# Performance work log

Measured on AMD Instinct MI355X. Metric: run time of the kernel, lower is better.

## Reference

```python
import jax, jax.numpy as jnp
import numpy as np

C = 128          # hidden_channels
N = 50000        # num nodes
E = 600000       # num edges
G = 256          # num graphs
PI = 3.141592653589793
EPS = 1e-5       # BatchNorm eps


def _lin(key, fan_in, fan_out):
    return jax.random.normal(key, (fan_in, fan_out), jnp.float32) / jnp.sqrt(fan_in)


def setup_inputs() -> dict:
    key = jax.random.key(0)
    ks = jax.random.split(key, 40)
    inp = {}
    inp["x"] = jax.random.normal(ks[0], (N, C), jnp.float32)
    inp["edge_index"] = jax.random.randint(ks[1], (2, E), 0, N)
    inp["edge_attr"] = jax.random.normal(ks[2], (E, C), jnp.float32)
    inp["batch"] = jnp.sort(jax.random.randint(ks[3], (N,), 0, G))
    # GATv2Conv 1
    inp["Wl1"] = _lin(ks[4], C, C); inp["bl1"] = jnp.zeros((C,), jnp.float32)
    inp["Wr1"] = _lin(ks[5], C, C); inp["br1"] = jnp.zeros((C,), jnp.float32)
    inp["We1"] = _lin(ks[6], C, C)
    inp["att1"] = jax.random.normal(ks[7], (C,), jnp.float32) / jnp.sqrt(C)
    inp["bo1"] = jnp.zeros((C,), jnp.float32)
    # GATv2Conv 2
    inp["Wl2"] = _lin(ks[8], C, C); inp["bl2"] = jnp.zeros((C,), jnp.float32)
    inp["Wr2"] = _lin(ks[9], C, C); inp["br2"] = jnp.zeros((C,), jnp.float32)
    inp["We2"] = _lin(ks[10], C, C)
    inp["att2"] = jax.random.normal(ks[11], (C,), jnp.float32) / jnp.sqrt(C)
    inp["bo2"] = jnp.zeros((C,), jnp.float32)
    # BatchNorms (affine)
    inp["g1"] = jnp.ones((C,), jnp.float32); inp["be1"] = jnp.zeros((C,), jnp.float32)
    inp["g2"] = jnp.ones((C,), jnp.float32); inp["be2"] = jnp.zeros((C,), jnp.float32)
    # AttentionalAggregation gate MLP (lin1 -> tanh -> lin2)
    inp["Ag1"] = _lin(ks[12], C, C); inp["bg1"] = jnp.zeros((C,), jnp.float32)
    inp["Ag2"] = _lin(ks[13], C, C); inp["bg2"] = jnp.zeros((C,), jnp.float32)
    # final Linear
    inp["Wf"] = _lin(ks[14], C, C); inp["bf"] = jnp.zeros((C,), jnp.float32)
    return inp


def gatv2(x, src, dst, ea, Wl, bl, Wr, br, We, att, bo):
    # add self-loops with fill_value='mean' (mean of incoming edge_attr per node)
    ones = jnp.ones(src.shape, x.dtype)
    deg = jax.ops.segment_sum(ones, dst, N)
    loop_attr = jax.ops.segment_sum(ea, dst, N) / jnp.maximum(deg, 1.0)[:, None]
    ar = jnp.arange(N)
    s = jnp.concatenate([src, ar])
    d = jnp.concatenate([dst, ar])
    ea_full = jnp.concatenate([ea, loop_attr], axis=0)  # [E+N, C]
    xl = x @ Wl + bl   # source transform
    xr = x @ Wr + br   # target transform
    m = xl[s] + xr[d] + ea_full @ We                    # [E+N, C]
    a = jnp.sum(jax.nn.leaky_relu(m, 0.2) * att, axis=-1)  # [E+N]
    # scatter-softmax over incoming edges of each target node
    amax = jax.ops.segment_max(a, d, N)
    ex = jnp.exp(a - amax[d])
    den = jax.ops.segment_sum(ex, d, N)
    alpha = ex / den[d]
    return jax.ops.segment_sum(alpha[:, None] * xl[s], d, N) + bo


def batchnorm(x, g, b):
    mu = x.mean(axis=0)
    var = x.var(axis=0)
    return (x - mu) * jax.lax.rsqrt(var + EPS) * g + b


def att_pool(x, batch, A1, b1, A2, b2):
    # gate_nn: lin1 -> tanh -> lin2, then per-graph per-feature softmax weights
    gate = jnp.tanh(x @ A1 + b1) @ A2 + b2              # [N, C]
    gmax = jax.ops.segment_max(gate, batch, G)
    eg = jnp.exp(gate - gmax[batch])
    den = jax.ops.segment_sum(eg, batch, G)
    w = eg / den[batch]
    return jax.ops.segment_sum(w * x, batch, G)          # [G, C]


def reference(x, edge_index, edge_attr, batch,
              Wl1, bl1, Wr1, br1, We1, att1, bo1,
              Wl2, bl2, Wr2, br2, We2, att2, bo2,
              g1, be1, g2, be2,
              Ag1, bg1, Ag2, bg2, Wf, bf):
    src, dst = edge_index[0], edge_index[1]
    h = gatv2(x, src, dst, edge_attr, Wl1, bl1, Wr1, br1, We1, att1, bo1)
    h = jnp.tanh(batchnorm(h, g1, be1))   # dropout = identity (eval)
    h = gatv2(h, src, dst, edge_attr, Wl2, bl2, Wr2, br2, We2, att2, bo2)
    h = jnp.tanh(batchnorm(h, g2, be2))
    p = att_pool(h, batch, Ag1, bg1, Ag2, bg2)           # [G, C]
    o = jnp.tanh(p @ Wf + bf)
    axis, aperture = jnp.split(o, 2, axis=-1)            # [G, C//2] each
    return axis * PI, (aperture + 1.0) * PI
```

## Files before the change

### kernel.cpp

```cpp
#include <hip/hip_runtime.h>
#include <hip/hip_bf16.h>
#include <math.h>

#define C 128
#define NN 50000
#define EE 600000
#define GG 256
#define PI_F 3.14159265358979323846f
#define EPS_BN 1e-5f
#define SCAN_G ((NN + 255) / 256)

typedef __attribute__((ext_vector_type(8)))  short  short8;
typedef __attribute__((ext_vector_type(16))) float  floatx16;
typedef __attribute__((ext_vector_type(4)))  float  float4v;
typedef __attribute__((ext_vector_type(4)))  unsigned short ushort4v;

static __device__ __forceinline__ short f2bs(float x) {
    union { float f; unsigned u; } v; v.f = x;
    unsigned r = v.u + 0x7FFF + ((v.u >> 16) & 1);
    return (short)(r >> 16);
}
static __device__ __forceinline__ float bs2f(unsigned short b) {
    union { unsigned u; float f; } v; v.u = (unsigned)b << 16; return v.f;
}

__global__ void k_cast(const float* __restrict__ in, unsigned short* __restrict__ out, int n4) {
    int i = blockIdx.x * blockDim.x + threadIdx.x;
    if (i < n4) {
        float4v v = ((const float4v*)in)[i];
        ushort4v o;
        o.x = (unsigned short)f2bs(v.x); o.y = (unsigned short)f2bs(v.y);
        o.z = (unsigned short)f2bs(v.z); o.w = (unsigned short)f2bs(v.w);
        ((ushort4v*)out)[i] = o;
    }
}

__global__ void k_prep(const float* __restrict__ W0, const float* __restrict__ W1,
                       const float* __restrict__ W2, const float* __restrict__ W3,
                       const float* __restrict__ W4, const float* __restrict__ W5,
                       const float* __restrict__ W6, const float* __restrict__ W7,
                       unsigned short* __restrict__ WT) {
    __shared__ short s[C * 136];
    const float* W;
    switch (blockIdx.x) {
        case 0: W = W0; break; case 1: W = W1; break;
        case 2: W = W2; break; case 3: W = W3; break;
        case 4: W = W4; break; case 5: W = W5; break;
        case 6: W = W6; break; default: W = W7; break;
    }
    for (int i = threadIdx.x; i < C * C; i += 256) {
        int k = i >> 7, n = i & (C - 1);
        s[n * 136 + k] = f2bs(W[i]);
    }
    __syncthreads();
    unsigned short* out = WT + (size_t)blockIdx.x * C * C;
    for (int i8 = threadIdx.x; i8 < C * C / 8; i8 += 256) {
        int n = i8 >> 4, k0 = (i8 & 15) * 8;
        *(short8*)(out + n * C + k0) = *(const short8*)&s[n * 136 + k0];
    }
}

static __device__ __forceinline__ void stage_wt(const unsigned short* __restrict__ WT, short* sWT) {
    for (int i8 = threadIdx.x; i8 < C * C / 8; i8 += 256) {
        int n = i8 >> 4, k0 = (i8 & 15) * 8;
        *(short8*)&sWT[n * 136 + k0] = *(const short8*)(WT + n * C + k0);
    }
}

__global__ void k_count(const int* __restrict__ dst, int* __restrict__ deg) {
    int e = blockIdx.x * blockDim.x + threadIdx.x;
    if (e < EE) atomicAdd(&deg[dst[e]], 1);
}

__global__ void k_scan1(const int* __restrict__ deg, int* __restrict__ bsum) {
    __shared__ int s[256];
    int t = threadIdx.x;
    int idx = blockIdx.x * 256 + t;
    s[t] = (idx < NN) ? deg[idx] : 0;
    __syncthreads();
    for (int off = 128; off > 0; off >>= 1) {
        if (t < off) s[t] += s[t + off];
        __syncthreads();
    }
    if (t == 0) bsum[blockIdx.x] = s[0];
}

__global__ void k_scan2(const int* __restrict__ bsum, int* __restrict__ boff, int* __restrict__ row_ptr) {
    __shared__ int s[256];
    int t = threadIdx.x;
    int v0 = (t < SCAN_G) ? bsum[t] : 0;
    s[t] = v0;
    __syncthreads();
    for (int off = 1; off < 256; off <<= 1) {
        int v = (t >= off) ? s[t - off] : 0;
        __syncthreads();
        s[t] += v;
        __syncthreads();
    }
    if (t < SCAN_G) boff[t] = s[t] - v0;
    if (t == 255) row_ptr[NN] = s[255];
}

__global__ void k_scan3(const int* __restrict__ deg, const int* __restrict__ boff,
                        int* __restrict__ row_ptr) {
    __shared__ int s[256];
    int t = threadIdx.x;
    int idx = blockIdx.x * 256 + t;
    int v = (idx < NN) ? deg[idx] : 0;
    s[t] = v;
    __syncthreads();
    for (int off = 1; off < 256; off <<= 1) {
        int u = (t >= off) ? s[t - off] : 0;
        __syncthreads();
        s[t] += u;
        __syncthreads();
    }
    if (idx < NN) row_ptr[idx] = boff[blockIdx.x] + s[t] - v;
}

__global__ void k_fill(const int* __restrict__ src, const int* __restrict__ dst,
                       const int* __restrict__ row_ptr, int* __restrict__ fill,
                       int* __restrict__ eid, int* __restrict__ scsr, int* __restrict__ dcsr) {
    int e = blockIdx.x * blockDim.x + threadIdx.x;
    if (e < EE) {
        int d = dst[e];
        int pos = atomicAdd(&fill[d], 1);
        int i = row_ptr[d] + pos;
        eid[i] = e;
        scsr[i] = src[e];
        dcsr[i] = d;
    }
}

__global__ void k_cast_esum(const float* __restrict__ ea, const int* __restrict__ eid,
                            const int* __restrict__ row_ptr,
                            unsigned short* __restrict__ ea_csr, unsigned short* __restrict__ esum) {
    int n = blockIdx.x; int c = threadIdx.x;
    int s = row_ptr[n], e = row_ptr[n + 1];
    float acc = 0.f;
    for (int i = s; i < e; i++) {
        float v = ea[(size_t)eid[i] * C + c];
        acc += v;
        ea_csr[(size_t)i * C + c] = (unsigned short)f2bs(v);
    }
    esum[(size_t)n * C + c] = (unsigned short)f2bs(acc / fmaxf((float)(e - s), 1.f));
}

template<bool TANH, bool OUT_BF16>
__launch_bounds__(256)
__global__ void k_gemm(const unsigned short* __restrict__ A, const unsigned short* __restrict__ WT,
                       const float* __restrict__ bias, void* __restrict__ outv, int M) {
    __shared__ short sWT[C * 136];
    stage_wt(WT, sWT);
    __syncthreads();

    int lane = threadIdx.x & 63;
    int wave = threadIdx.x >> 6;
    int m    = lane & 31;
    int half = lane >> 5;
    int row0 = blockIdx.x * 128 + wave * 32;
    int rowA = row0 + m;
    int rowC = (rowA < M) ? rowA : (M - 1);
    const unsigned short* rp = A + (size_t)rowC * C;

    floatx16 acc[4];
    #pragma unroll
    for (int t = 0; t < 4; ++t)
        #pragma unroll
        for (int r = 0; r < 16; ++r) acc[t][r] = 0.f;

    #pragma unroll
    for (int s = 0; s < 8; ++s) {
        int k0 = s * 16 + half * 8;
        short8 af = *(const short8*)(rp + k0);
        #pragma unroll
        for (int t = 0; t < 4; ++t) {
            short8 bfr = *(const short8*)(&sWT[(t * 32 + m) * 136 + k0]);
            acc[t] = __builtin_amdgcn_mfma_f32_32x32x16_bf16(af, bfr, acc[t], 0, 0, 0);
        }
    }

    #pragma unroll
    for (int t = 0; t < 4; ++t) {
        int n = t * 32 + m;
        float b = bias ? bias[n] : 0.f;
        #pragma unroll
        for (int r = 0; r < 16; ++r) {
            int rl  = (r & 3) + 8 * (r >> 2) + 4 * half;
            int row = row0 + rl;
            if (row < M) {
                float v = acc[t][r] + b;
                if (TANH) v = tanhf(v);
                if (OUT_BF16) ((unsigned short*)outv)[(size_t)row * C + n] = (unsigned short)f2bs(v);
                else          ((float*)outv)[(size_t)row * C + n] = v;
            }
        }
    }
}

__launch_bounds__(256)
__global__ void k_gemm2(const unsigned short* __restrict__ A,
                        const unsigned short* __restrict__ WT0, const float* __restrict__ b0,
                        const unsigned short* __restrict__ WT1, const float* __restrict__ b1,
                        unsigned short* __restrict__ out0, unsigned short* __restrict__ out1,
                        int M) {
    __shared__ short sWT[C * 136];
    int lane = threadIdx.x & 63;
    int wave = threadIdx.x >> 6;
    int m    = lane & 31;
    int half = lane >> 5;
    int row0 = blockIdx.x * 128 + wave * 32;
    int rowA = row0 + m;
    int rowC = (rowA < M) ? rowA : (M - 1);
    const unsigned short* rp = A + (size_t)rowC * C;

    short8 af[8];
    #pragma unroll
    for (int s = 0; s < 8; ++s) af[s] = *(const short8*)(rp + s * 16 + half * 8);

    for (int phase = 0; phase < 2; ++phase) {
        const unsigned short* WT = phase ? WT1 : WT0;
        const float* bb = phase ? b1 : b0;
        unsigned short* out = phase ? out1 : out0;
        if (phase) __syncthreads();
        stage_wt(WT, sWT);
        __syncthreads();

        floatx16 acc[4];
        #pragma unroll
        for (int t = 0; t < 4; ++t)
            #pragma unroll
            for (int r = 0; r < 16; ++r) acc[t][r] = 0.f;

        #pragma unroll
        for (int s = 0; s < 8; ++s) {
            int k0 = s * 16 + half * 8;
            #pragma unroll
            for (int t = 0; t < 4; ++t) {
                short8 bfr = *(const short8*)(&sWT[(t * 32 + m) * 136 + k0]);
                acc[t] = __builtin_amdgcn_mfma_f32_32x32x16_bf16(af[s], bfr, acc[t], 0, 0, 0);
            }
        }

        #pragma unroll
        for (int t = 0; t < 4; ++t) {
            int n = t * 32 + m;
            float b = bb[n];
            #pragma unroll
            for (int r = 0; r < 16; ++r) {
                int rl  = (r & 3) + 8 * (r >> 2) + 4 * half;
                int row = row0 + rl;
                if (row < M)
                    out[(size_t)row * C + n] = (unsigned short)f2bs(acc[t][r] + b);
            }
        }
    }
}

template<bool SELF>
__launch_bounds__(256)
__global__ void k_gemm_logit(const unsigned short* __restrict__ A, const unsigned short* __restrict__ WT,
                             const unsigned short* __restrict__ xl, const unsigned short* __restrict__ xr,
                             const int* __restrict__ scsr, const int* __restrict__ dcsr,
                             const float* __restrict__ att, float* __restrict__ aout, int M) {
    __shared__ short sWT[C * 136];
    stage_wt(WT, sWT);
    __syncthreads();

    int lane = threadIdx.x & 63;
    int wave = threadIdx.x >> 6;
    int m    = lane & 31;
    int half = lane >> 5;
    int row0 = blockIdx.x * 128 + wave * 32;
    int rowA = row0 + m;
    int rowC = (rowA < M) ? rowA : (M - 1);
    const unsigned short* rp = A + (size_t)rowC * C;

    floatx16 acc[4];
    #pragma unroll
    for (int t = 0; t < 4; ++t)
        #pragma unroll
        for (int r = 0; r < 16; ++r) acc[t][r] = 0.f;

    #pragma unroll
    for (int s = 0; s < 8; ++s) {
        int k0 = s * 16 + half * 8;
        short8 af = *(const short8*)(rp + k0);
        #pragma unroll
        for (int t = 0; t < 4; ++t) {
            short8 bfr = *(const short8*)(&sWT[(t * 32 + m) * 136 + k0]);
            acc[t] = __builtin_amdgcn_mfma_f32_32x32x16_bf16(af, bfr, acc[t], 0, 0, 0);
        }
    }

    float attv[4];
    #pragma unroll
    for (int t = 0; t < 4; ++t) attv[t] = att[t * 32 + m];

    #pragma unroll
    for (int r = 0; r < 16; ++r) {
        int rl  = (r & 3) + 8 * (r >> 2) + 4 * half;
        int row = row0 + rl;
        int rc  = (row < M) ? row : (M - 1);
        int si, di;
        if (SELF) { si = rc; di = rc; }
        else      { si = scsr[rc]; di = dcsr[rc]; }
        const unsigned short* xls = xl + (size_t)si * C;
        const unsigned short* xrs = xr + (size_t)di * C;
        float p = 0.f;
        #pragma unroll
        for (int t = 0; t < 4; ++t) {
            int col = t * 32 + m;
            float v = acc[t][r] + bs2f(xls[col]) + bs2f(xrs[col]);
            v = (v >= 0.f) ? v : 0.2f * v;
            p = fmaf(v, attv[t], p);
        }
        p += __shfl_xor(p, 1);  p += __shfl_xor(p, 2);  p += __shfl_xor(p, 4);
        p += __shfl_xor(p, 8);  p += __shfl_xor(p, 16);
        if (m == 0 && row < M) aout[row] = p;
    }
}

__global__ void k_attn(const unsigned short* __restrict__ xl, const float* __restrict__ a,
                       const int* __restrict__ row_ptr, const int* __restrict__ scsr,
                       const float* __restrict__ bo, float* __restrict__ out) {
    int n = blockIdx.x * 4 + (threadIdx.x >> 6);
    int lane = threadIdx.x & 63;
    if (n >= NN) return;
    int s = row_ptr[n], e = row_ptr[n + 1];
    float aself = a[EE + n];
    float mx = aself;
    for (int i = s + lane; i < e; i += 64) mx = fmaxf(mx, a[i]);
    #pragma unroll
    for (int o = 1; o < 64; o <<= 1) mx = fmaxf(mx, __shfl_xor(mx, o));
    float part = (lane == 0) ? expf(aself - mx) : 0.f;
    for (int i = s + lane; i < e; i += 64) part += expf(a[i] - mx);
    #pragma unroll
    for (int o = 1; o < 64; o <<= 1) part += __shfl_xor(part, o);
    float inv = 1.f / part;

    int sub = lane >> 4;
    int cb  = (lane & 15) * 8;
    float acc[8];
    #pragma unroll
    for (int j = 0; j < 8; ++j) acc[j] = 0.f;

    if (sub == 0) {
        float w = expf(aself - mx) * inv;
        short8 v = *(const short8*)(xl + (size_t)n * C + cb);
        #pragma unroll
        for (int j = 0; j < 8; ++j) acc[j] = w * bs2f((unsigned short)v[j]);
    }

    for (int i = s + sub; i < e; i += 4) {
        float w = expf(a[i] - mx) * inv;
        int sd = scsr[i];
        short8 v = *(const short8*)(xl + (size_t)sd * C + cb);
        #pragma unroll
        for (int j = 0; j < 8; ++j) acc[j] = fmaf(w, bs2f((unsigned short)v[j]), acc[j]);
    }

    #pragma unroll
    for (int j = 0; j < 8; ++j) {
        acc[j] += __shfl_xor(acc[j], 16);
        acc[j] += __shfl_xor(acc[j], 32);
    }
    if (sub == 0) {
        float* op = out + (size_t)n * C + cb;
        float4v o0, o1;
        o0.x = acc[0] + bo[cb + 0]; o0.y = acc[1] + bo[cb + 1];
        o0.z = acc[2] + bo[cb + 2]; o0.w = acc[3] + bo[cb + 3];
        o1.x = acc[4] + bo[cb + 4]; o1.y = acc[5] + bo[cb + 5];
        o1.z = acc[6] + bo[cb + 6]; o1.w = acc[7] + bo[cb + 7];
        ((float4v*)op)[0] = o0;
        ((float4v*)op)[1] = o1;
    }
}

__launch_bounds__(1024)
__global__ void k_bnstats(const float* __restrict__ v, float* __restrict__ sums) {
    __shared__ float r1[8][C], r2[8][C];
    int c = threadIdx.x & (C - 1);
    int q = threadIdx.x >> 7;
    float s1 = 0.f, s2 = 0.f;
    for (int n = blockIdx.x * 8 + q; n < NN; n += 8 * gridDim.x) {
        float x = v[(size_t)n * C + c]; s1 += x; s2 += x * x;
    }
    r1[q][c] = s1; r2[q][c] = s2;
    __syncthreads();
    if (threadIdx.x < C) {
        float a1 = 0.f, a2 = 0.f;
        #pragma unroll
        for (int k = 0; k < 8; ++k) { a1 += r1[k][c]; a2 += r2[k][c]; }
        atomicAdd(&sums[c], a1); atomicAdd(&sums[C + c], a2);
    }
}

__global__ void k_bnapply(const float* __restrict__ v, const float* __restrict__ sums,
                          const float* __restrict__ g, const float* __restrict__ b,
                          unsigned short* __restrict__ h) {
    int i4 = blockIdx.x * blockDim.x + threadIdx.x;
    if (i4 >= NN * C / 4) return;
    int c0 = (i4 * 4) & (C - 1);
    float4v x = ((const float4v*)v)[i4];
    ushort4v o;
    #pragma unroll
    for (int j = 0; j < 4; ++j) {
        int c = c0 + j;
        float mu  = sums[c] * (1.f / NN);
        float var = sums[C + c] * (1.f / NN) - mu * mu;
        float r = rsqrtf(var + EPS_BN);
        o[j] = (unsigned short)f2bs(tanhf((x[j] - mu) * r * g[c] + b[c]));
    }
    ((ushort4v*)h)[i4] = o;
}

__global__ void k_bounds(const int* __restrict__ batch, int* __restrict__ gs, int* __restrict__ ge) {
    int n = blockIdx.x * blockDim.x + threadIdx.x;
    if (n >= NN) return;
    int b = batch[n];
    if (n == 0 || batch[n - 1] != b) gs[b] = n;
    if (n == NN - 1 || batch[n + 1] != b) ge[b] = n + 1;
}

__launch_bounds__(1024)
__global__ void k_poolfinal(const unsigned short* __restrict__ gate, const unsigned short* __restrict__ h,
                            const int* __restrict__ gs, const int* __restrict__ ge,
                            const float* __restrict__ Wf, const float* __restrict__ bf,
                            float* __restrict__ out) {
    __shared__ float sm[8][C], sden[8][C], sacc[8][C];
    __shared__ float row[C];
    int g = blockIdx.x;
    int t = threadIdx.x;
    int c = t & (C - 1);
    int q = t >> 7;
    int s = gs[g], e = ge[g];
    float m = -1e30f, den = 0.f, acc = 0.f;
    for (int n = s + q; n < e; n += 8) {
        float gv = bs2f(gate[(size_t)n * C + c]);
        float hv = bs2f(h[(size_t)n * C + c]);
        float mn = fmaxf(m, gv);
        float sc = expf(m - mn);
        float w  = expf(gv - mn);
        den = den * sc + w;
        acc = acc * sc + w * hv;
        m = mn;
    }
    sm[q][c] = m; sden[q][c] = den; sacc[q][c] = acc;
    __syncthreads();
    if (t < C) {
        float M = sm[0][c];
        #pragma unroll
        for (int k = 1; k < 8; ++k) M = fmaxf(M, sm[k][c]);
        float D = 0.f, A = 0.f;
        #pragma unroll
        for (int k = 0; k < 8; ++k) {
            float al = expf(sm[k][c] - M);
            D += sden[k][c] * al;
            A += sacc[k][c] * al;
        }
        row[c] = (e > s) ? A / D : 0.f;
    }
    __syncthreads();
    float p = 0.f;
    #pragma unroll
    for (int kk = 0; kk < 16; ++kk) {
        int k = q * 16 + kk;
        p = fmaf(row[k], Wf[k * C + c], p);
    }
    sden[q][c] = p;
    __syncthreads();
    if (t < C) {
        float accf = bf[c];
        #pragma unroll
        for (int k = 0; k < 8; ++k) accf += sden[k][c];
        float o = tanhf(accf);
        if (c < C / 2) out[g * (C / 2) + c] = o * PI_F;
        else out[GG * (C / 2) + g * (C / 2) + (c - C / 2)] = (o + 1.f) * PI_F;
    }
}

extern "C" void kernel_launch(void* const* d_in, const int* in_sizes, int n_in,
                              void* d_out, int out_size, void* d_ws, size_t ws_size,
                              hipStream_t stream) {
    const float* x   = (const float*)d_in[0];
    const int*   ei  = (const int*)d_in[1];
    const float* ea  = (const float*)d_in[2];
    const int* batch = (const int*)d_in[3];
    const float *Wl1 = (const float*)d_in[4],  *bl1 = (const float*)d_in[5];
    const float *Wr1 = (const float*)d_in[6],  *br1 = (const float*)d_in[7];
    const float *We1 = (const float*)d_in[8],  *att1 = (const float*)d_in[9], *bo1 = (const float*)d_in[10];
    const float *Wl2 = (const float*)d_in[11], *bl2 = (const float*)d_in[12];
    const float *Wr2 = (const float*)d_in[13], *br2 = (const float*)d_in[14];
    const float *We2 = (const float*)d_in[15], *att2 = (const float*)d_in[16], *bo2 = (const float*)d_in[17];
    const float *g1  = (const float*)d_in[18], *be1 = (const float*)d_in[19];
    const float *g2  = (const float*)d_in[20], *be2 = (const float*)d_in[21];
    const float *Ag1 = (const float*)d_in[22], *bg1 = (const float*)d_in[23];
    const float *Ag2 = (const float*)d_in[24], *bg2 = (const float*)d_in[25];
    const float *Wf  = (const float*)d_in[26], *bf  = (const float*)d_in[27];
    const int* src = ei; const int* dst = ei + EE;

    char* wsb = (char*)d_ws;
    size_t off = 0;
    auto alloc = [&](size_t bytes) -> char* {
        char* p = wsb + off; off += (bytes + 255) & ~(size_t)255; return p;
    };
    unsigned short* ea_u  = (unsigned short*)alloc((size_t)EE * C * 2);
    unsigned short* x_u   = (unsigned short*)alloc((size_t)NN * C * 2);
    unsigned short* xl_u  = (unsigned short*)alloc((size_t)NN * C * 2);
    unsigned short* xr_u  = (unsigned short*)alloc((size_t)NN * C * 2);
    unsigned short* h_u   = (unsigned short*)alloc((size_t)NN * C * 2);
    unsigned short* es_u  = (unsigned short*)alloc((size_t)NN * C * 2);
    unsigned short* WTall = (unsigned short*)alloc((size_t)8 * C * C * 2);
    float* aggf  = (float*)alloc((size_t)NN * C * 4);
    float* a     = (float*)alloc((size_t)(EE + NN) * 4);
    int*   csrz  = (int*)alloc((size_t)2 * NN * 4);
    int* deg = csrz, *fill = csrz + NN;
    int* row_ptr = (int*)alloc((size_t)(NN + 1) * 4);
    int* eid     = (int*)alloc((size_t)EE * 4);
    int* scsr    = (int*)alloc((size_t)EE * 4);
    int* dcsr    = (int*)alloc((size_t)EE * 4);
    float* sums  = (float*)alloc(4 * C * 4);
    int* gbounds = (int*)alloc(2 * GG * 4);
    int* gs = gbounds, *ge = gbounds + GG;
    int* bscan   = (int*)alloc((size_t)2 * SCAN_G * 4);
    int* bsum = bscan, *boff = bscan + SCAN_G;

    hipMemsetAsync(csrz,    0, (size_t)2 * NN * 4, stream);
    hipMemsetAsync(sums,    0, 4 * C * 4, stream);
    hipMemsetAsync(gbounds, 0, 2 * GG * 4, stream);

    const size_t WSZ = (size_t)C * C;
    const unsigned short *WTl1 = WTall + 0 * WSZ, *WTr1 = WTall + 1 * WSZ, *WTe1 = WTall + 2 * WSZ;
    const unsigned short *WTl2 = WTall + 3 * WSZ, *WTr2 = WTall + 4 * WSZ, *WTe2 = WTall + 5 * WSZ;
    const unsigned short *WTA1 = WTall + 6 * WSZ, *WTA2 = WTall + 7 * WSZ;

    k_prep<<<8, 256, 0, stream>>>(Wl1, Wr1, We1, Wl2, Wr2, We2, Ag1, Ag2, WTall);
    k_cast<<<(NN * C / 4 + 255) / 256, 256, 0, stream>>>(x, x_u, NN * C / 4);
    k_count<<<(EE + 255) / 256, 256, 0, stream>>>(dst, deg);
    k_scan1<<<SCAN_G, 256, 0, stream>>>(deg, bsum);
    k_scan2<<<1, 256, 0, stream>>>(bsum, boff, row_ptr);
    k_scan3<<<SCAN_G, 256, 0, stream>>>(deg, boff, row_ptr);
    k_fill<<<(EE + 255) / 256, 256, 0, stream>>>(src, dst, row_ptr, fill, eid, scsr, dcsr);
    k_cast_esum<<<NN, C, 0, stream>>>(ea, eid, row_ptr, ea_u, es_u);

    int gN = (NN + 127) / 128, gE = (EE + 127) / 128;

    k_gemm2<<<gN, 256, 0, stream>>>(x_u, WTl1, bl1, WTr1, br1, xl_u, xr_u, NN);
    k_gemm_logit<true ><<<gN, 256, 0, stream>>>(es_u, WTe1, xl_u, xr_u, nullptr, nullptr, att1, a + EE, NN);
    k_gemm_logit<false><<<gE, 256, 0, stream>>>(ea_u, WTe1, xl_u, xr_u, scsr, dcsr, att1, a, EE);
    k_attn<<<(NN + 3) / 4, 256, 0, stream>>>(xl_u, a, row_ptr, scsr, bo1, aggf);
    k_bnstats<<<256, 1024, 0, stream>>>(aggf, sums);
    k_bnapply<<<(NN * C / 4 + 255) / 256, 256, 0, stream>>>(aggf, sums, g1, be1, h_u);

    k_gemm2<<<gN, 256, 0, stream>>>(h_u, WTl2, bl2, WTr2, br2, xl_u, xr_u, NN);
    k_gemm_logit<true ><<<gN, 256, 0, stream>>>(es_u, WTe2, xl_u, xr_u, nullptr, nullptr, att2, a + EE, NN);
    k_gemm_logit<false><<<gE, 256, 0, stream>>>(ea_u, WTe2, xl_u, xr_u, scsr, dcsr, att2, a, EE);
    k_attn<<<(NN + 3) / 4, 256, 0, stream>>>(xl_u, a, row_ptr, scsr, bo2, aggf);
    k_bnstats<<<256, 1024, 0, stream>>>(aggf, sums + 2 * C);
    k_bnapply<<<(NN * C / 4 + 255) / 256, 256, 0, stream>>>(aggf, sums + 2 * C, g2, be2, h_u);

    k_gemm<true,  true><<<gN, 256, 0, stream>>>(h_u,  WTA1, bg1, xl_u, NN);
    k_gemm<false, true><<<gN, 256, 0, stream>>>(xl_u, WTA2, bg2, xr_u, NN);
    k_bounds<<<(NN + 255) / 256, 256, 0, stream>>>(batch, gs, ge);
    k_poolfinal<<<GG, 1024, 0, stream>>>(xr_u, h_u, gs, ge, Wf, bf, (float*)d_out);
}
```

Baseline: 1.131 ms.

## Fuse BN apply into GEMMs, fuse gate MLP, merge scans, split edge cast

```diff
diff --git a/kernel.cpp b/kernel.cpp
--- a/kernel.cpp
+++ b/kernel.cpp
@@ -85,11 +85,11 @@
     if (t == 0) bsum[blockIdx.x] = s[0];
 }
 
-__global__ void k_scan2(const int* __restrict__ bsum, int* __restrict__ boff, int* __restrict__ row_ptr) {
+__global__ void k_scan3(const int* __restrict__ deg, const int* __restrict__ bsum,
+                        int* __restrict__ row_ptr) {
     __shared__ int s[256];
     int t = threadIdx.x;
-    int v0 = (t < SCAN_G) ? bsum[t] : 0;
-    s[t] = v0;
+    s[t] = (t < SCAN_G) ? bsum[t] : 0;
     __syncthreads();
     for (int off = 1; off < 256; off <<= 1) {
         int v = (t >= off) ? s[t - off] : 0;
@@ -97,14 +97,9 @@
         s[t] += v;
         __syncthreads();
     }
-    if (t < SCAN_G) boff[t] = s[t] - v0;
-    if (t == 255) row_ptr[NN] = s[255];
-}
-
-__global__ void k_scan3(const int* __restrict__ deg, const int* __restrict__ boff,
-                        int* __restrict__ row_ptr) {
-    __shared__ int s[256];
-    int t = threadIdx.x;
+    int boffI = (blockIdx.x > 0) ? s[blockIdx.x - 1] : 0;
+    if (blockIdx.x == SCAN_G - 1 && t == 0) row_ptr[NN] = s[SCAN_G - 1];
+    __syncthreads();
     int idx = blockIdx.x * 256 + t;
     int v = (idx < NN) ? deg[idx] : 0;
     s[t] = v;
@@ -115,7 +110,7 @@
         s[t] += u;
         __syncthreads();
     }
-    if (idx < NN) row_ptr[idx] = boff[blockIdx.x] + s[t] - v;
+    if (idx < NN) row_ptr[idx] = boffI + s[t] - v;
 }
 
 __global__ void k_fill(const int* __restrict__ src, const int* __restrict__ dst,
@@ -132,74 +127,60 @@
     }
 }
 
-__global__ void k_cast_esum(const float* __restrict__ ea, const int* __restrict__ eid,
-                            const int* __restrict__ row_ptr,
-                            unsigned short* __restrict__ ea_csr, unsigned short* __restrict__ esum) {
-    int n = blockIdx.x; int c = threadIdx.x;
+__global__ void k_cast_perm(const float* __restrict__ ea, const int* __restrict__ eid,
+                            unsigned short* __restrict__ out) {
+    int i = blockIdx.x * 4 + (threadIdx.x >> 6);
+    int lane = threadIdx.x & 63;
+    if (i >= EE) return;
+    int e = eid[i];
+    const float2* rp = (const float2*)(ea + (size_t)e * C);
+    float2 v = rp[lane];
+    unsigned pk = (unsigned)(unsigned short)f2bs(v.x) | ((unsigned)(unsigned short)f2bs(v.y) << 16);
+    ((unsigned*)(out + (size_t)i * C))[lane] = pk;
+}
+
+__global__ void k_esum(const unsigned short* __restrict__ ea_csr, const int* __restrict__ row_ptr,
+                       unsigned short* __restrict__ esum) {
+    int n = blockIdx.x * 2 + (threadIdx.x >> 7);
+    int c = threadIdx.x & (C - 1);
+    if (n >= NN) return;
     int s = row_ptr[n], e = row_ptr[n + 1];
     float acc = 0.f;
-    for (int i = s; i < e; i++) {
-        float v = ea[(size_t)eid[i] * C + c];
-        acc += v;
-        ea_csr[(size_t)i * C + c] = (unsigned short)f2bs(v);
-    }
+    for (int i = s; i < e; i++) acc += bs2f(ea_csr[(size_t)i * C + c]);
     esum[(size_t)n * C + c] = (unsigned short)f2bs(acc / fmaxf((float)(e - s), 1.f));
 }
 
-template<bool TANH, bool OUT_BF16>
+static __device__ __forceinline__ short8 bn_load8(const float* __restrict__ rp, int k0,
+                                                  const float* __restrict__ sums,
+                                                  const float* __restrict__ gg,
+                                                  const float* __restrict__ bbn) {
+    float4v x0 = *(const float4v*)(rp + k0);
+    float4v x1 = *(const float4v*)(rp + k0 + 4);
+    short8 t;
+    #pragma unroll
+    for (int j = 0; j < 4; ++j) {
+        int c = k0 + j;
+        float mu  = sums[c] * (1.f / NN);
+        float var = sums[C + c] * (1.f / NN) - mu * mu;
+        float r = rsqrtf(var + EPS_BN);
+        t[j] = f2bs(tanhf((x0[j] - mu) * r * gg[c] + bbn[c]));
+    }
+    #pragma unroll
+    for (int j = 0; j < 4; ++j) {
+        int c = k0 + 4 + j;
+        float mu  = sums[c] * (1.f / NN);
+        float var = sums[C + c] * (1.f / NN) - mu * mu;
+        float r = rsqrtf(var + EPS_BN);
+        t[4 + j] = f2bs(tanhf((x1[j] - mu) * r * gg[c] + bbn[c]));
+    }
+    return t;
+}
+
+template<bool BN_A>
 __launch_bounds__(256)
-__global__ void k_gemm(const unsigned short* __restrict__ A, const unsigned short* __restrict__ WT,
-                       const float* __restrict__ bias, void* __restrict__ outv, int M) {
-    __shared__ short sWT[C * 136];
-    stage_wt(WT, sWT);
-    __syncthreads();
-
-    int lane = threadIdx.x & 63;
-    int wave = threadIdx.x >> 6;
-    int m    = lane & 31;
-    int half = lane >> 5;
-    int row0 = blockIdx.x * 128 + wave * 32;
-    int rowA = row0 + m;
-    int rowC = (rowA < M) ? rowA : (M - 1);
-    const unsigned short* rp = A + (size_t)rowC * C;
-
-    floatx16 acc[4];
-    #pragma unroll
-    for (int t = 0; t < 4; ++t)
-        #pragma unroll
-        for (int r = 0; r < 16; ++r) acc[t][r] = 0.f;
-
-    #pragma unroll
-    for (int s = 0; s < 8; ++s) {
-        int k0 = s * 16 + half * 8;
-        short8 af = *(const short8*)(rp + k0);
-        #pragma unroll
-        for (int t = 0; t < 4; ++t) {
-            short8 bfr = *(const short8*)(&sWT[(t * 32 + m) * 136 + k0]);
-            acc[t] = __builtin_amdgcn_mfma_f32_32x32x16_bf16(af, bfr, acc[t], 0, 0, 0);
-        }
-    }
-
-    #pragma unroll
-    for (int t = 0; t < 4; ++t) {
-        int n = t * 32 + m;
-        float b = bias ? bias[n] : 0.f;
-        #pragma unroll
-        for (int r = 0; r < 16; ++r) {
-            int rl  = (r & 3) + 8 * (r >> 2) + 4 * half;
-            int row = row0 + rl;
-            if (row < M) {
-                float v = acc[t][r] + b;
-                if (TANH) v = tanhf(v);
-                if (OUT_BF16) ((unsigned short*)outv)[(size_t)row * C + n] = (unsigned short)f2bs(v);
-                else          ((float*)outv)[(size_t)row * C + n] = v;
-            }
-        }
-    }
-}
-
-__launch_bounds__(256)
-__global__ void k_gemm2(const unsigned short* __restrict__ A,
+__global__ void k_gemm2(const void* __restrict__ Ap,
+                        const float* __restrict__ sums, const float* __restrict__ gg,
+                        const float* __restrict__ bbn,
                         const unsigned short* __restrict__ WT0, const float* __restrict__ b0,
                         const unsigned short* __restrict__ WT1, const float* __restrict__ b1,
                         unsigned short* __restrict__ out0, unsigned short* __restrict__ out1,
@@ -212,11 +193,17 @@
     int row0 = blockIdx.x * 128 + wave * 32;
     int rowA = row0 + m;
     int rowC = (rowA < M) ? rowA : (M - 1);
-    const unsigned short* rp = A + (size_t)rowC * C;
 
     short8 af[8];
-    #pragma unroll
-    for (int s = 0; s < 8; ++s) af[s] = *(const short8*)(rp + s * 16 + half * 8);
+    if (BN_A) {
+        const float* rp = ((const float*)Ap) + (size_t)rowC * C;
+        #pragma unroll
+        for (int s = 0; s < 8; ++s) af[s] = bn_load8(rp, s * 16 + half * 8, sums, gg, bbn);
+    } else {
+        const unsigned short* rp = ((const unsigned short*)Ap) + (size_t)rowC * C;
+        #pragma unroll
+        for (int s = 0; s < 8; ++s) af[s] = *(const short8*)(rp + s * 16 + half * 8);
+    }
 
     for (int phase = 0; phase < 2; ++phase) {
         const unsigned short* WT = phase ? WT1 : WT0;
@@ -271,53 +258,56 @@
     int wave = threadIdx.x >> 6;
     int m    = lane & 31;
     int half = lane >> 5;
-    int row0 = blockIdx.x * 128 + wave * 32;
-    int rowA = row0 + m;
-    int rowC = (rowA < M) ? rowA : (M - 1);
-    const unsigned short* rp = A + (size_t)rowC * C;
-
-    floatx16 acc[4];
-    #pragma unroll
-    for (int t = 0; t < 4; ++t)
-        #pragma unroll
-        for (int r = 0; r < 16; ++r) acc[t][r] = 0.f;
-
-    #pragma unroll
-    for (int s = 0; s < 8; ++s) {
-        int k0 = s * 16 + half * 8;
-        short8 af = *(const short8*)(rp + k0);
-        #pragma unroll
-        for (int t = 0; t < 4; ++t) {
-            short8 bfr = *(const short8*)(&sWT[(t * 32 + m) * 136 + k0]);
-            acc[t] = __builtin_amdgcn_mfma_f32_32x32x16_bf16(af, bfr, acc[t], 0, 0, 0);
-        }
-    }
 
     float attv[4];
     #pragma unroll
     for (int t = 0; t < 4; ++t) attv[t] = att[t * 32 + m];
 
-    #pragma unroll
-    for (int r = 0; r < 16; ++r) {
-        int rl  = (r & 3) + 8 * (r >> 2) + 4 * half;
-        int row = row0 + rl;
-        int rc  = (row < M) ? row : (M - 1);
-        int si, di;
-        if (SELF) { si = rc; di = rc; }
-        else      { si = scsr[rc]; di = dcsr[rc]; }
-        const unsigned short* xls = xl + (size_t)si * C;
-        const unsigned short* xrs = xr + (size_t)di * C;
-        float p = 0.f;
-        #pragma unroll
-        for (int t = 0; t < 4; ++t) {
-            int col = t * 32 + m;
-            float v = acc[t][r] + bs2f(xls[col]) + bs2f(xrs[col]);
-            v = (v >= 0.f) ? v : 0.2f * v;
-            p = fmaf(v, attv[t], p);
-        }
-        p += __shfl_xor(p, 1);  p += __shfl_xor(p, 2);  p += __shfl_xor(p, 4);
-        p += __shfl_xor(p, 8);  p += __shfl_xor(p, 16);
-        if (m == 0 && row < M) aout[row] = p;
+    for (int rt = 0; rt < 2; ++rt) {
+        int row0 = blockIdx.x * 256 + rt * 128 + wave * 32;
+        int rowA = row0 + m;
+        int rowC = (rowA < M) ? rowA : (M - 1);
+        const unsigned short* rp = A + (size_t)rowC * C;
+
+        floatx16 acc[4];
+        #pragma unroll
+        for (int t = 0; t < 4; ++t)
+            #pragma unroll
+            for (int r = 0; r < 16; ++r) acc[t][r] = 0.f;
+
+        #pragma unroll
+        for (int s = 0; s < 8; ++s) {
+            int k0 = s * 16 + half * 8;
+            short8 af = *(const short8*)(rp + k0);
+            #pragma unroll
+            for (int t = 0; t < 4; ++t) {
+                short8 bfr = *(const short8*)(&sWT[(t * 32 + m) * 136 + k0]);
+                acc[t] = __builtin_amdgcn_mfma_f32_32x32x16_bf16(af, bfr, acc[t], 0, 0, 0);
+            }
+        }
+
+        #pragma unroll
+        for (int r = 0; r < 16; ++r) {
+            int rl  = (r & 3) + 8 * (r >> 2) + 4 * half;
+            int row = row0 + rl;
+            int rc  = (row < M) ? row : (M - 1);
+            int si, di;
+            if (SELF) { si = rc; di = rc; }
+            else      { si = scsr[rc]; di = dcsr[rc]; }
+            const unsigned short* xls = xl + (size_t)si * C;
+            const unsigned short* xrs = xr + (size_t)di * C;
+            float p = 0.f;
+            #pragma unroll
+            for (int t = 0; t < 4; ++t) {
+                int col = t * 32 + m;
+                float v = acc[t][r] + bs2f(xls[col]) + bs2f(xrs[col]);
+                v = (v >= 0.f) ? v : 0.2f * v;
+                p = fmaf(v, attv[t], p);
+            }
+            p += __shfl_xor(p, 1);  p += __shfl_xor(p, 2);  p += __shfl_xor(p, 4);
+            p += __shfl_xor(p, 8);  p += __shfl_xor(p, 16);
+            if (m == 0 && row < M) aout[row] = p;
+        }
     }
 }
 
@@ -396,31 +386,107 @@
     }
 }
 
-__global__ void k_bnapply(const float* __restrict__ v, const float* __restrict__ sums,
-                          const float* __restrict__ g, const float* __restrict__ b,
-                          unsigned short* __restrict__ h) {
-    int i4 = blockIdx.x * blockDim.x + threadIdx.x;
-    if (i4 >= NN * C / 4) return;
-    int c0 = (i4 * 4) & (C - 1);
-    float4v x = ((const float4v*)v)[i4];
-    ushort4v o;
-    #pragma unroll
-    for (int j = 0; j < 4; ++j) {
-        int c = c0 + j;
-        float mu  = sums[c] * (1.f / NN);
-        float var = sums[C + c] * (1.f / NN) - mu * mu;
-        float r = rsqrtf(var + EPS_BN);
-        o[j] = (unsigned short)f2bs(tanhf((x[j] - mu) * r * g[c] + b[c]));
-    }
-    ((ushort4v*)h)[i4] = o;
-}
-
 __global__ void k_bounds(const int* __restrict__ batch, int* __restrict__ gs, int* __restrict__ ge) {
     int n = blockIdx.x * blockDim.x + threadIdx.x;
     if (n >= NN) return;
     int b = batch[n];
     if (n == 0 || batch[n - 1] != b) gs[b] = n;
     if (n == NN - 1 || batch[n + 1] != b) ge[b] = n + 1;
+}
+
+__launch_bounds__(256)
+__global__ void k_gate(const float* __restrict__ aggf,
+                       const float* __restrict__ sums, const float* __restrict__ gg,
+                       const float* __restrict__ bbn,
+                       const unsigned short* __restrict__ WT1, const float* __restrict__ bg1,
+                       const unsigned short* __restrict__ WT2, const float* __restrict__ bg2,
+                       unsigned short* __restrict__ hout, unsigned short* __restrict__ gate,
+                       int M) {
+    __shared__ short sW[C * 136];
+    __shared__ short sT[128 * 136];
+    stage_wt(WT1, sW);
+
+    int lane = threadIdx.x & 63;
+    int wave = threadIdx.x >> 6;
+    int m    = lane & 31;
+    int half = lane >> 5;
+    int row0 = blockIdx.x * 128 + wave * 32;
+    int rowA = row0 + m;
+    int rowC = (rowA < M) ? rowA : (M - 1);
+    const float* rp = aggf + (size_t)rowC * C;
+
+    short8 af[8];
+    #pragma unroll
+    for (int s = 0; s < 8; ++s) {
+        int k0 = s * 16 + half * 8;
+        af[s] = bn_load8(rp, k0, sums, gg, bbn);
+        if (rowA < M) *(short8*)(hout + (size_t)rowA * C + k0) = af[s];
+    }
+    __syncthreads();
+
+    floatx16 acc[4];
+    #pragma unroll
+    for (int t = 0; t < 4; ++t)
+        #pragma unroll
+        for (int r = 0; r < 16; ++r) acc[t][r] = 0.f;
+
+    #pragma unroll
+    for (int s = 0; s < 8; ++s) {
+        int k0 = s * 16 + half * 8;
+        #pragma unroll
+        for (int t = 0; t < 4; ++t) {
+            short8 bfr = *(const short8*)(&sW[(t * 32 + m) * 136 + k0]);
+            acc[t] = __builtin_amdgcn_mfma_f32_32x32x16_bf16(af[s], bfr, acc[t], 0, 0, 0);
+        }
+    }
+
+    #pragma unroll
+    for (int t = 0; t < 4; ++t) {
+        int n = t * 32 + m;
+        float b = bg1[n];
+        #pragma unroll
+        for (int r = 0; r < 16; ++r) {
+            int rl  = (r & 3) + 8 * (r >> 2) + 4 * half;
+            int lrow = wave * 32 + rl;
+            sT[lrow * 136 + n] = f2bs(tanhf(acc[t][r] + b));
+        }
+    }
+    __syncthreads();
+    stage_wt(WT2, sW);
+    __syncthreads();
+
+    short8 af2[8];
+    #pragma unroll
+    for (int s = 0; s < 8; ++s)
+        af2[s] = *(const short8*)&sT[(wave * 32 + m) * 136 + s * 16 + half * 8];
+
+    #pragma unroll
+    for (int t = 0; t < 4; ++t)
+        #pragma unroll
+        for (int r = 0; r < 16; ++r) acc[t][r] = 0.f;
+
+    #pragma unroll
+    for (int s = 0; s < 8; ++s) {
+        int k0 = s * 16 + half * 8;
+        #pragma unroll
+        for (int t = 0; t < 4; ++t) {
+            short8 bfr = *(const short8*)(&sW[(t * 32 + m) * 136 + k0]);
+            acc[t] = __builtin_amdgcn_mfma_f32_32x32x16_bf16(af2[s], bfr, acc[t], 0, 0, 0);
+        }
+    }
+
+    #pragma unroll
+    for (int t = 0; t < 4; ++t) {
+        int n = t * 32 + m;
+        float b = bg2[n];
+        #pragma unroll
+        for (int r = 0; r < 16; ++r) {
+            int rl  = (r & 3) + 8 * (r >> 2) + 4 * half;
+            int row = row0 + rl;
+            if (row < M)
+                gate[(size_t)row * C + n] = (unsigned short)f2bs(acc[t][r] + b);
+        }
+    }
 }
 
 __launch_bounds__(1024)
@@ -523,8 +589,7 @@
     float* sums  = (float*)alloc(4 * C * 4);
     int* gbounds = (int*)alloc(2 * GG * 4);
     int* gs = gbounds, *ge = gbounds + GG;
-    int* bscan   = (int*)alloc((size_t)2 * SCAN_G * 4);
-    int* bsum = bscan, *boff = bscan + SCAN_G;
+    int* bscan   = (int*)alloc((size_t)SCAN_G * 4);
 
     hipMemsetAsync(csrz,    0, (size_t)2 * NN * 4, stream);
     hipMemsetAsync(sums,    0, 4 * C * 4, stream);
@@ -538,30 +603,31 @@
     k_prep<<<8, 256, 0, stream>>>(Wl1, Wr1, We1, Wl2, Wr2, We2, Ag1, Ag2, WTall);
     k_cast<<<(NN * C / 4 + 255) / 256, 256, 0, stream>>>(x, x_u, NN * C / 4);
     k_count<<<(EE + 255) / 256, 256, 0, stream>>>(dst, deg);
-    k_scan1<<<SCAN_G, 256, 0, stream>>>(deg, bsum);
-    k_scan2<<<1, 256, 0, stream>>>(bsum, boff, row_ptr);
-    k_scan3<<<SCAN_G, 256, 0, stream>>>(deg, boff, row_ptr);
+    k_scan1<<<SCAN_G, 256, 0, stream>>>(deg, bscan);
+    k_scan3<<<SCAN_G, 256, 0, stream>>>(deg, bscan, row_ptr);
     k_fill<<<(EE + 255) / 256, 256, 0, stream>>>(src, dst, row_ptr, fill, eid, scsr, dcsr);
-    k_cast_esum<<<NN, C, 0, stream>>>(ea, eid, row_ptr, ea_u, es_u);
-
-    int gN = (NN + 127) / 128, gE = (EE + 127) / 128;
-
-    k_gemm2<<<gN, 256, 0, stream>>>(x_u, WTl1, bl1, WTr1, br1, xl_u, xr_u, NN);
-    k_gemm_logit<true ><<<gN, 256, 0, stream>>>(es_u, WTe1, xl_u, xr_u, nullptr, nullptr, att1, a + EE, NN);
-    k_gemm_logit<false><<<gE, 256, 0, stream>>>(ea_u, WTe1, xl_u, xr_u, scsr, dcsr, att1, a, EE);
+    k_cast_perm<<<(EE + 3) / 4, 256, 0, stream>>>(ea, eid, ea_u);
+    k_esum<<<(NN + 1) / 2, 256, 0, stream>>>(ea_u, row_ptr, es_u);
+
+    int gN = (NN + 127) / 128;
+    int gN2 = (NN + 255) / 256, gE2 = (EE + 255) / 256;
+
+    k_gemm2<false><<<gN, 256, 0, stream>>>(x_u, nullptr, nullptr, nullptr,
+                                           WTl1, bl1, WTr1, br1, xl_u, xr_u, NN);
+    k_gemm_logit<true ><<<gN2, 256, 0, stream>>>(es_u, WTe1, xl_u, xr_u, nullptr, nullptr, att1, a + EE, NN);
+    k_gemm_logit<false><<<gE2, 256, 0, stream>>>(ea_u, WTe1, xl_u, xr_u, scsr, dcsr, att1, a, EE);
     k_attn<<<(NN + 3) / 4, 256, 0, stream>>>(xl_u, a, row_ptr, scsr, bo1, aggf);
     k_bnstats<<<256, 1024, 0, stream>>>(aggf, sums);
-    k_bnapply<<<(NN * C / 4 + 255) / 256, 256, 0, stream>>>(aggf, sums, g1, be1, h_u);
-
-    k_gemm2<<<gN, 256, 0, stream>>>(h_u, WTl2, bl2, WTr2, br2, xl_u, xr_u, NN);
-    k_gemm_logit<true ><<<gN, 256, 0, stream>>>(es_u, WTe2, xl_u, xr_u, nullptr, nullptr, att2, a + EE, NN);
-    k_gemm_logit<false><<<gE, 256, 0, stream>>>(ea_u, WTe2, xl_u, xr_u, scsr, dcsr, att2, a, EE);
+
+    k_gemm2<true ><<<gN, 256, 0, stream>>>(aggf, sums, g1, be1,
+                                           WTl2, bl2, WTr2, br2, xl_u, xr_u, NN);
+    k_gemm_logit<true ><<<gN2, 256, 0, stream>>>(es_u, WTe2, xl_u, xr_u, nullptr, nullptr, att2, a + EE, NN);
+    k_gemm_logit<false><<<gE2, 256, 0, stream>>>(ea_u, WTe2, xl_u, xr_u, scsr, dcsr, att2, a, EE);
     k_attn<<<(NN + 3) / 4, 256, 0, stream>>>(xl_u, a, row_ptr, scsr, bo2, aggf);
     k_bnstats<<<256, 1024, 0, stream>>>(aggf, sums + 2 * C);
-    k_bnapply<<<(NN * C / 4 + 255) / 256, 256, 0, stream>>>(aggf, sums + 2 * C, g2, be2, h_u);
-
-    k_gemm<true,  true><<<gN, 256, 0, stream>>>(h_u,  WTA1, bg1, xl_u, NN);
-    k_gemm<false, true><<<gN, 256, 0, stream>>>(xl_u, WTA2, bg2, xr_u, NN);
+
+    k_gate<<<gN, 256, 0, stream>>>(aggf, sums + 2 * C, g2, be2,
+                                   WTA1, bg1, WTA2, bg2, h_u, xr_u, NN);
     k_bounds<<<(NN + 255) / 256, 256, 0, stream>>>(batch, gs, ge);
     k_poolfinal<<<GG, 1024, 0, stream>>>(xr_u, h_u, gs, ge, Wf, bf, (float*)d_out);
 }
```

Result: slower. 1.300 ms (+14.9%).
